# Kernel tuning notes

Hardware: AMD Instinct MI355X
Metric: run time of the kernel (lower is better)

Reference implementation:

```python
import jax, jax.numpy as jnp
import numpy as np

N, C, T, H, W = 2, 512, 8, 28, 28
THW = T * H * W
BN_EPS = 1e-5


def conv1x1(x, Wt, b):
    # pointwise channel mixing, equivalent to 1x1 Conv2d/Conv3d on (N,C,T,H,W)
    return jnp.einsum('oc,ncthw->nothw', Wt, x) + b[None, :, None, None, None]


def setup_inputs() -> dict:
    key = jax.random.key(0)
    ks = jax.random.split(key, 8)
    s = 1.0 / np.sqrt(C)
    x = jax.random.normal(ks[0], (N, C, T, H, W), dtype=jnp.float32)
    mask = jax.random.uniform(ks[1], (N, C, T, H, W), dtype=jnp.float32)
    Wh = jax.random.normal(ks[2], (C, C), dtype=jnp.float32) * s
    Wg = jax.random.normal(ks[3], (C, C), dtype=jnp.float32) * s
    Wm = jax.random.normal(ks[4], (C, C), dtype=jnp.float32) * s
    Wz = jax.random.normal(ks[5], (C, C), dtype=jnp.float32) * s  # kaiming-like
    bh = jnp.zeros((C,), jnp.float32)
    bg = jnp.zeros((C,), jnp.float32)
    bm = jnp.zeros((C,), jnp.float32)
    bz = jnp.zeros((C,), jnp.float32)
    bn_w = jnp.ones((C,), jnp.float32)
    bn_b = jnp.zeros((C,), jnp.float32)
    gamma = jnp.float32(1.0)  # self.gamma (undefined in source __init__); learnable scalar
    return dict(x=x, mask=mask, Wh=Wh, bh=bh, Wg=Wg, bg=bg, Wm=Wm, bm=bm,
                Wz=Wz, bz=bz, bn_w=bn_w, bn_b=bn_b, gamma=gamma)


def reference(x, mask, Wh, bh, Wg, bg, Wm, bm, Wz, bz, bn_w, bn_b, gamma):
    n = x.shape[0]
    # proj_f = h(x) reshaped (N, THW, C); proj_g = g(x) (N, C, THW)
    ph_x = conv1x1(x, Wh, bh).reshape(n, C, THW)
    pg = conv1x1(x, Wg, bg).reshape(n, C, THW)
    # energy[n,t,s] = sum_c ph_x[n,c,t] * pg[n,c,s]  -> (N, THW, THW)
    energy = jnp.einsum('nct,ncs->nts', ph_x, pg)
    attention = jax.nn.softmax(energy, axis=-1)
    # proj_h uses self.h on mask (faithful to source)
    ph_m = conv1x1(mask, Wh, bh).reshape(n, C, THW)
    # bmm(proj_h, attention^T): [n,c,t] = sum_s ph_m[n,c,s] * attention[n,t,s]
    mask_energy = jnp.einsum('ncs,nts->nct', ph_m, attention)
    mask_atten = jax.nn.softmax(mask_energy, axis=-1)  # softmax over THW
    pm = conv1x1(x, Wm, bm)
    out = pm * mask_atten.reshape(n, C, T, H, W)
    # W_z: 1x1 Conv3d + BatchNorm3d (training-mode batch stats, weight=1, bias=0)
    wy = conv1x1(x, Wz, bz)
    mu = jnp.mean(wy, axis=(0, 2, 3, 4), keepdims=True)
    var = jnp.var(wy, axis=(0, 2, 3, 4), keepdims=True)
    wy = (wy - mu) * jax.lax.rsqrt(var + BN_EPS)
    wy = wy * bn_w[None, :, None, None, None] + bn_b[None, :, None, None, None]
    return gamma * out + wy
```

## Files before the change

### kernel.cpp

```cpp
#include <hip/hip_runtime.h>
#include <hip/hip_bf16.h>
#include <math.h>

#define NN 2
#define CC 512
#define PP 6272
#define TCHMAX 1664
#define NCHK 4
#define NJT 49
#define KSP 4
#define EM 64.0f
static const size_t PPC = (size_t)PP * CC;
static const size_t NCP = (size_t)NN * PPC;

typedef unsigned short ushortT;
typedef __attribute__((ext_vector_type(8))) short short8;
typedef __attribute__((ext_vector_type(4))) float f32x4;

__device__ __forceinline__ ushortT f2bf(float f) {
  __hip_bfloat16 h = __float2bfloat16(f);
  return *reinterpret_cast<ushortT*>(&h);
}
__device__ __forceinline__ float bf2f(ushortT u) {
  return __uint_as_float(((unsigned)u) << 16);
}

__device__ __forceinline__ void ld_g2l(const void* g, void* l) {
  __builtin_amdgcn_global_load_lds(
      (const __attribute__((address_space(1))) void*)g,
      (__attribute__((address_space(3))) void*)l, 16, 0, 0);
}

__global__ __launch_bounds__(256) void k_cast4(const float* __restrict__ W0,
                                               const float* __restrict__ W1,
                                               const float* __restrict__ W2,
                                               const float* __restrict__ W3,
                                               ushortT* __restrict__ dst) {
  const float* src = (blockIdx.y == 0) ? W0 : (blockIdx.y == 1) ? W1
                    : (blockIdx.y == 2) ? W2 : W3;
  const int i = (blockIdx.x * 256 + threadIdx.x) * 4;
  float4 v = *(const float4*)&src[i];
  ushort4 o;
  o.x = f2bf(v.x); o.y = f2bf(v.y); o.z = f2bf(v.z); o.w = f2bf(v.w);
  *(ushort4*)&dst[(size_t)blockIdx.y * CC * CC + i] = o;
}

__global__ void k_castT(const float* __restrict__ in, ushortT* __restrict__ out) {
  __shared__ float T[32][33];
  const int p0 = blockIdx.x * 32, c0 = blockIdx.y * 32;
  const int tx = threadIdx.x, ty = threadIdx.y;
  const size_t nbi = (size_t)blockIdx.z * PPC;
#pragma unroll
  for (int i = 0; i < 4; ++i)
    T[ty + i * 8][tx] = in[nbi + (size_t)(c0 + ty + i * 8) * PP + p0 + tx];
  __syncthreads();
#pragma unroll
  for (int i = 0; i < 4; ++i) {
    int r = ty + i * 8;
    out[nbi + (size_t)(p0 + r) * CC + c0 + tx] = f2bf(T[tx][r]);
  }
}

template <int OM>
__global__ __launch_bounds__(256) void k_bgemm(const ushortT* __restrict__ A,
                                               const ushortT* __restrict__ B,
                                               const float* __restrict__ bias,
                                               ushortT* __restrict__ out,
                                               int KD, size_t sAn, size_t sBn,
                                               size_t sOn, int ldo) {
  __shared__ __align__(16) ushortT smem[17408];
  ushortT* At = smem;
  ushortT* Bt = smem + 8192;
  const int tid = threadIdx.x;
  const int l = tid & 63, w = tid >> 6;
  const int j0 = blockIdx.x * 128;
  const int i0 = blockIdx.y * 128;
  A += (size_t)blockIdx.z * sAn;
  B += (size_t)blockIdx.z * sBn;
  out += (size_t)blockIdx.z * sOn;
  const int wi = (w & 1) * 64, wj = (w >> 1) * 64;
  const int lr = l & 15, lk = l >> 4;
  const int sr = l >> 3, scg = l & 7;

  f32x4 acc[4][4] = {};

  for (int k0 = 0; k0 < KD; k0 += 64) {
#pragma unroll
    for (int i = 0; i < 4; ++i) {
      int row = w * 32 + i * 8 + sr;
      int cs = scg ^ (row & 7);
      ld_g2l(A + (size_t)(i0 + row) * KD + k0 + cs * 8, (char*)At + (w * 4 + i) * 1024);
      ld_g2l(B + (size_t)(j0 + row) * KD + k0 + cs * 8, (char*)Bt + (w * 4 + i) * 1024);
    }
    __syncthreads();
#pragma unroll
    for (int ks = 0; ks < 2; ++ks) {
      short8 af[4], bfv[4];
      const int cc = ks * 4 + lk;
#pragma unroll
      for (int tt = 0; tt < 4; ++tt) {
        int row = wi + tt * 16 + lr;
        af[tt] = *(const short8*)((const char*)At + row * 128 + ((cc ^ (row & 7)) * 16));
      }
#pragma unroll
      for (int ss = 0; ss < 4; ++ss) {
        int row = wj + ss * 16 + lr;
        bfv[ss] = *(const short8*)((const char*)Bt + row * 128 + ((cc ^ (row & 7)) * 16));
      }
#pragma unroll
      for (int tt = 0; tt < 4; ++tt)
#pragma unroll
        for (int ss = 0; ss < 4; ++ss)
          acc[tt][ss] = __builtin_amdgcn_mfma_f32_16x16x32_bf16(af[tt], bfv[ss], acc[tt][ss], 0, 0, 0);
    }
    __syncthreads();
  }
  const int r4 = (l >> 4) * 4;
  ushortT (*Tr)[136] = (ushortT(*)[136])smem;
  if (OM == 0) {
    float bj[4];
#pragma unroll
    for (int ss = 0; ss < 4; ++ss) bj[ss] = bias[j0 + wj + ss * 16 + lr];
#pragma unroll
    for (int tt = 0; tt < 4; ++tt)
#pragma unroll
      for (int r = 0; r < 4; ++r) {
        int row = wi + tt * 16 + r4 + r;
#pragma unroll
        for (int ss = 0; ss < 4; ++ss)
          Tr[row][wj + ss * 16 + lr] = f2bf(acc[tt][ss][r] + bj[ss]);
      }
  } else {
#pragma unroll
    for (int tt = 0; tt < 4; ++tt)
#pragma unroll
      for (int r = 0; r < 4; ++r) {
        int row = wi + tt * 16 + r4 + r;
        float bi = bias[i0 + row];
#pragma unroll
        for (int ss = 0; ss < 4; ++ss)
          Tr[row][wj + ss * 16 + lr] = f2bf(acc[tt][ss][r] + bi);
      }
  }
  __syncthreads();
#pragma unroll
  for (int q = 0; q < 8; ++q) {
    int chunk = q * 256 + tid;
    int row = chunk >> 4, cg = chunk & 15;
    short8 v = *(const short8*)&Tr[row][cg * 8];
    *(short8*)&out[(size_t)(i0 + row) * ldo + j0 + cg * 8] = v;
  }
}

__global__ __launch_bounds__(256) void k_energy(const ushortT* __restrict__ phxT,
                                                const ushortT* __restrict__ pgT,
                                                ushortT* __restrict__ Ech,
                                                float* __restrict__ Estat,
                                                int tbase) {
  __shared__ __align__(16) ushortT smem[17408];
  __shared__ float Ss[128][2];
  ushortT* At = smem;
  ushortT* Bt = smem + 8192;
  const int tid = threadIdx.x;
  const int l = tid & 63, w = tid >> 6;
  const int j0 = blockIdx.x * 128;
  const int i0 = blockIdx.y * 128;
  const int z = blockIdx.z;
  const ushortT* A = phxT + (size_t)z * PPC + (size_t)tbase * CC;
  const ushortT* B = pgT + (size_t)z * PPC;
  ushortT* out = Ech + (size_t)z * TCHMAX * PP;
  const int wi = (w & 1) * 64, wj = (w >> 1) * 64;
  const int lr = l & 15, lk = l >> 4;
  const int sr = l >> 3, scg = l & 7;

  f32x4 acc[4][4] = {};

  for (int k0 = 0; k0 < CC; k0 += 64) {
#pragma unroll
    for (int i = 0; i < 4; ++i) {
      int row = w * 32 + i * 8 + sr;
      int cs = scg ^ (row & 7);
      ld_g2l(A + (size_t)(i0 + row) * CC + k0 + cs * 8, (char*)At + (w * 4 + i) * 1024);
      ld_g2l(B + (size_t)(j0 + row) * CC + k0 + cs * 8, (char*)Bt + (w * 4 + i) * 1024);
    }
    __syncthreads();
#pragma unroll
    for (int ks = 0; ks < 2; ++ks) {
      short8 af[4], bfv[4];
      const int cc = ks * 4 + lk;
#pragma unroll
      for (int tt = 0; tt < 4; ++tt) {
        int row = wi + tt * 16 + lr;
        af[tt] = *(const short8*)((const char*)At + row * 128 + ((cc ^ (row & 7)) * 16));
      }
#pragma unroll
      for (int ss = 0; ss < 4; ++ss) {
        int row = wj + ss * 16 + lr;
        bfv[ss] = *(const short8*)((const char*)Bt + row * 128 + ((cc ^ (row & 7)) * 16));
      }
#pragma unroll
      for (int tt = 0; tt < 4; ++tt)
#pragma unroll
        for (int ss = 0; ss < 4; ++ss)
          acc[tt][ss] = __builtin_amdgcn_mfma_f32_16x16x32_bf16(af[tt], bfv[ss], acc[tt][ss], 0, 0, 0);
    }
    __syncthreads();
  }
  const int r4 = (l >> 4) * 4;
  const int jh = w >> 1;
  ushortT (*Tr)[136] = (ushortT(*)[136])smem;
#pragma unroll
  for (int tt = 0; tt < 4; ++tt)
#pragma unroll
    for (int r = 0; r < 4; ++r) {
      int row = wi + tt * 16 + r4 + r;
      float u0 = __expf(acc[tt][0][r] - EM);
      float u1 = __expf(acc[tt][1][r] - EM);
      float u2 = __expf(acc[tt][2][r] - EM);
      float u3 = __expf(acc[tt][3][r] - EM);
      Tr[row][wj + lr]      = f2bf(u0);
      Tr[row][wj + 16 + lr] = f2bf(u1);
      Tr[row][wj + 32 + lr] = f2bf(u2);
      Tr[row][wj + 48 + lr] = f2bf(u3);
      float sx = (u0 + u1) + (u2 + u3);
#pragma unroll
      for (int d = 1; d < 16; d <<= 1) sx += __shfl_xor(sx, d);
      if (lr == 0) Ss[row][jh] = sx;
    }
  __syncthreads();
  if (tid < 128) {
    Estat[((size_t)z * TCHMAX + i0 + tid) * NJT + blockIdx.x] =
        Ss[tid][0] + Ss[tid][1];
  }
#pragma unroll
  for (int q = 0; q < 8; ++q) {
    int chunk = q * 256 + tid;
    int row = chunk >> 4, cg = chunk & 15;
    short8 v = *(const short8*)&Tr[row][cg * 8];
    *(short8*)&out[(size_t)(i0 + row) * PP + j0 + cg * 8] = v;
  }
}

__global__ __launch_bounds__(256) void k_zcomb(const float* __restrict__ Estat,
                                               float* __restrict__ rowZ, int rows) {
  const int r = blockIdx.x * 256 + threadIdx.x;
  if (r >= NN * rows) return;
  const int z = r / rows, tl = r % rows;
  const float* p = Estat + ((size_t)z * TCHMAX + tl) * NJT;
  float s = 0.f;
#pragma unroll
  for (int j = 0; j < NJT; ++j) s += p[j];
  rowZ[z * TCHMAX + tl] = 1.0f / s;
}

__global__ __launch_bounds__(256) void k_me(const ushortT* __restrict__ phmB,
                                            const ushortT* __restrict__ Ech,
                                            ushortT* __restrict__ mePart) {
  __shared__ __align__(16) ushortT smem[12288];
  ushortT* At = smem;
  ushortT* Bt = smem + 8192;
  const int tid = threadIdx.x;
  const int l = tid & 63, w = tid >> 6;
  const int tl0 = blockIdx.x * 64;
  const int c0 = blockIdx.y * 128;
  const int bz = blockIdx.z;
  const int z = bz / KSP, ks = bz % KSP;
  const size_t nb = (size_t)z * PPC;
  const ushortT* Pb = Ech + (size_t)z * TCHMAX * PP;
  const int wc = (w & 1) * 64, wt = (w >> 1) * 32;
  const int lr = l & 15, lk = l >> 4;
  const int sr = l >> 3, scg = l & 7;

  f32x4 acc[4][2] = {};

  const int sBeg = ((ks * 98) / KSP) * 64;
  const int sEnd = (((ks + 1) * 98) / KSP) * 64;
  for (int s0 = sBeg; s0 < sEnd; s0 += 64) {
#pragma unroll
    for (int i = 0; i < 4; ++i) {
      int row = w * 32 + i * 8 + sr;
      int cs = scg ^ (row & 7);
      ld_g2l(phmB + nb + (size_t)(c0 + row) * PP + s0 + cs * 8,
             (char*)At + (w * 4 + i) * 1024);
    }
#pragma unroll
    for (int i = 0; i < 2; ++i) {
      int row = w * 16 + i * 8 + sr;
      int cs = scg ^ (row & 7);
      ld_g2l(Pb + (size_t)(tl0 + row) * PP + s0 + cs * 8,
             (char*)Bt + (w * 2 + i) * 1024);
    }
    __syncthreads();
#pragma unroll
    for (int kk = 0; kk < 2; ++kk) {
      short8 af[4], bfv[2];
      const int cc = kk * 4 + lk;
#pragma unroll
      for (int ct = 0; ct < 4; ++ct) {
        int row = wc + ct * 16 + lr;
        af[ct] = *(const short8*)((const char*)At + row * 128 + ((cc ^ (row & 7)) * 16));
      }
#pragma unroll
      for (int tt = 0; tt < 2; ++tt) {
        int row = wt + tt * 16 + lr;
        bfv[tt] = *(const short8*)((const char*)Bt + row * 128 + ((cc ^ (row & 7)) * 16));
      }
#pragma unroll
      for (int ct = 0; ct < 4; ++ct)
#pragma unroll
        for (int tt = 0; tt < 2; ++tt)
          acc[ct][tt] = __builtin_amdgcn_mfma_f32_16x16x32_bf16(af[ct], bfv[tt], acc[ct][tt], 0, 0, 0);
    }
    __syncthreads();
  }
  const int r4 = (l >> 4) * 4;
  ushortT (*Tr)[72] = (ushortT(*)[72])smem;
#pragma unroll
  for (int ct = 0; ct < 4; ++ct)
#pragma unroll
    for (int r = 0; r < 4; ++r) {
      int row = wc + ct * 16 + r4 + r;
#pragma unroll
      for (int tt = 0; tt < 2; ++tt)
        Tr[row][wt + tt * 16 + lr] = f2bf(acc[ct][tt][r]);
    }
  __syncthreads();
  ushortT* out = mePart + ((size_t)(ks * NN + z) * CC) * TCHMAX;
#pragma unroll
  for (int q = 0; q < 4; ++q) {
    int chunk = q * 256 + tid;
    int row = chunk >> 3, cg = chunk & 7;
    short8 v = *(const short8*)&Tr[row][cg * 8];
    *(short8*)&out[(size_t)(c0 + row) * TCHMAX + tl0 + cg * 8] = v;
  }
}

__global__ __launch_bounds__(256) void k_meadd(const ushortT* __restrict__ mePart,
                                               const float* __restrict__ rowZ,
                                               ushortT* __restrict__ meb,
                                               int tbase, int rows) {
  const int idx = (blockIdx.x * 256 + threadIdx.x) * 4;
  const int tl = idx % rows;
  const int c = (idx / rows) % CC;
  const int z = idx / (rows * CC);
  float s0 = 0.f, s1 = 0.f, s2 = 0.f, s3 = 0.f;
#pragma unroll
  for (int ks = 0; ks < KSP; ++ks) {
    const size_t o = ((size_t)(ks * NN + z) * CC + c) * TCHMAX + tl;
    ushort4 a = *(const ushort4*)&mePart[o];
    s0 += bf2f(a.x); s1 += bf2f(a.y); s2 += bf2f(a.z); s3 += bf2f(a.w);
  }
  const float4 rz = *(const float4*)&rowZ[z * TCHMAX + tl];
  ushort4 v;
  v.x = f2bf(s0 * rz.x); v.y = f2bf(s1 * rz.y);
  v.z = f2bf(s2 * rz.z); v.w = f2bf(s3 * rz.w);
  *(ushort4*)&meb[((size_t)z * CC + c) * PP + tbase + tl] = v;
}

__global__ __launch_bounds__(256) void k_soft2(const ushortT* __restrict__ me,
                                               float* __restrict__ m2,
                                               float* __restrict__ Z2) {
  __shared__ float red[256];
  const ushortT* row = me + (size_t)blockIdx.x * PP;
  const int tid = threadIdx.x;
  const int NCH = PP / 8;
  float m = -INFINITY;
  for (int i = tid; i < NCH; i += 256) {
    short8 v = *(const short8*)&row[i * 8];
#pragma unroll
    for (int j = 0; j < 8; ++j) m = fmaxf(m, bf2f((ushortT)v[j]));
  }
  red[tid] = m;
  __syncthreads();
  for (int s = 128; s > 0; s >>= 1) {
    if (tid < s) red[tid] = fmaxf(red[tid], red[tid + s]);
    __syncthreads();
  }
  m = red[0];
  __syncthreads();
  float zz = 0.f;
  for (int i = tid; i < NCH; i += 256) {
    short8 v = *(const short8*)&row[i * 8];
#pragma unroll
    for (int j = 0; j < 8; ++j) zz += __expf(bf2f((ushortT)v[j]) - m);
  }
  red[tid] = zz;
  __syncthreads();
  for (int s = 128; s > 0; s >>= 1) {
    if (tid < s) red[tid] += red[tid + s];
    __syncthreads();
  }
  if (tid == 0) { m2[blockIdx.x] = m; Z2[blockIdx.x] = red[0]; }
}

__global__ __launch_bounds__(256) void k_bnstat(const ushortT* __restrict__ wz,
                                                float* __restrict__ mu,
                                                float* __restrict__ rinv) {
  __shared__ float rs[256];
  __shared__ float rq[256];
  const int c = blockIdx.x;
  const int tid = threadIdx.x;
  const int NCH = PP / 8;
  float s = 0.f, q = 0.f;
  for (int n = 0; n < NN; ++n) {
    const ushortT* rowp = wz + (size_t)n * CC * PP + (size_t)c * PP;
    for (int i = tid; i < NCH; i += 256) {
      short8 v = *(const short8*)&rowp[i * 8];
#pragma unroll
      for (int j = 0; j < 8; ++j) {
        float f = bf2f((ushortT)v[j]);
        s += f;
        q += f * f;
      }
    }
  }
  rs[tid] = s; rq[tid] = q;
  __syncthreads();
  for (int st = 128; st > 0; st >>= 1) {
    if (tid < st) { rs[tid] += rs[tid + st]; rq[tid] += rq[tid + st]; }
    __syncthreads();
  }
  if (tid == 0) {
    const float inv_n = 1.0f / (float)(NN * PP);
    float mean = rs[0] * inv_n;
    float var = rq[0] * inv_n - mean * mean;
    mu[c] = mean;
    rinv[c] = rsqrtf(var + 1e-5f);
  }
}

__global__ __launch_bounds__(256) void k_final(const ushortT* __restrict__ pmB,
                                               const ushortT* __restrict__ me,
                                               const ushortT* __restrict__ wz,
                                               const float* __restrict__ m2,
                                               const float* __restrict__ Z2,
                                               const float* __restrict__ mu,
                                               const float* __restrict__ rinv,
                                               const float* __restrict__ bnw,
                                               const float* __restrict__ bnb,
                                               const float* __restrict__ gamma,
                                               float* __restrict__ out) {
  const int e4 = blockIdx.x * 256 + threadIdx.x;
  const size_t e = (size_t)e4 * 4;
  const int nc = (int)(e / PP);
  const int c = nc & (CC - 1);
  const float m = m2[nc];
  const float rz = 1.0f / Z2[nc];
  const float mub = mu[c];
  const float ri = rinv[c] * bnw[c];
  const float bb = bnb[c];
  const float g = gamma[0];
  ushort4 pv = *(const ushort4*)&pmB[e];
  ushort4 mev = *(const ushort4*)&me[e];
  ushort4 wzv = *(const ushort4*)&wz[e];
  float4 o;
  o.x = g * bf2f(pv.x) * (__expf(bf2f(mev.x) - m) * rz) + (bf2f(wzv.x) - mub) * ri + bb;
  o.y = g * bf2f(pv.y) * (__expf(bf2f(mev.y) - m) * rz) + (bf2f(wzv.y) - mub) * ri + bb;
  o.z = g * bf2f(pv.z) * (__expf(bf2f(mev.z) - m) * rz) + (bf2f(wzv.z) - mub) * ri + bb;
  o.w = g * bf2f(pv.w) * (__expf(bf2f(mev.w) - m) * rz) + (bf2f(wzv.w) - mub) * ri + bb;
  *(float4*)&out[e] = o;
}

extern "C" void kernel_launch(void* const* d_in, const int* in_sizes, int n_in,
                              void* d_out, int out_size, void* d_ws, size_t ws_size,
                              hipStream_t stream) {
  (void)in_sizes; (void)n_in; (void)out_size; (void)ws_size;
  const float* x    = (const float*)d_in[0];
  const float* mask = (const float*)d_in[1];
  const float* Wh   = (const float*)d_in[2];
  const float* bh   = (const float*)d_in[3];
  const float* Wg   = (const float*)d_in[4];
  const float* bg   = (const float*)d_in[5];
  const float* Wm   = (const float*)d_in[6];
  const float* bm   = (const float*)d_in[7];
  const float* Wz   = (const float*)d_in[8];
  const float* bz   = (const float*)d_in[9];
  const float* bnw  = (const float*)d_in[10];
  const float* bnb  = (const float*)d_in[11];
  const float* gam  = (const float*)d_in[12];

  ushortT* wzb  = (ushortT*)d_ws;
  ushortT* meb  = wzb + NCP;
  ushortT* pmB  = meb + NCP;
  ushortT* phxT = pmB + NCP;
  ushortT* pgT  = phxT + NCP;
  ushortT* phmB = pgT + NCP;
  ushortT* Wbf  = phmB + NCP;
  ushortT* Whbf = Wbf;
  ushortT* Wgbf = Wbf + 1 * CC * CC;
  ushortT* Wmbf = Wbf + 2 * CC * CC;
  ushortT* Wzbf = Wbf + 3 * CC * CC;
  float* m2    = (float*)(Wbf + 4 * CC * CC);
  float* Z2    = m2 + NN * CC;
  float* mu    = Z2 + NN * CC;
  float* rin   = mu + CC;
  float* Estat = rin + CC;
  float* rowZ  = Estat + (size_t)NN * TCHMAX * NJT;
  float* region = rowZ + (size_t)NN * TCHMAX + 16;
  ushortT* xT    = (ushortT*)region;
  ushortT* maskT = xT + NCP;
  ushortT* Ech    = (ushortT*)region;
  ushortT* mePart = Ech + (size_t)NN * TCHMAX * PP;

  k_cast4<<<dim3(256, 4), 256, 0, stream>>>(Wh, Wg, Wm, Wz, Wbf);
  dim3 gct(PP / 32, CC / 32, NN);
  k_castT<<<gct, dim3(32, 8), 0, stream>>>(x, xT);
  k_castT<<<gct, dim3(32, 8), 0, stream>>>(mask, maskT);

  dim3 gPc(CC / 128, PP / 128, NN);
  k_bgemm<0><<<gPc, 256, 0, stream>>>(xT, Whbf, bh, phxT, CC, PPC, 0, PPC, CC);
  k_bgemm<0><<<gPc, 256, 0, stream>>>(xT, Wgbf, bg, pgT, CC, PPC, 0, PPC, CC);
  dim3 gCp(PP / 128, CC / 128, NN);
  k_bgemm<1><<<gCp, 256, 0, stream>>>(Whbf, maskT, bh, phmB, CC, 0, PPC, PPC, PP);
  k_bgemm<1><<<gCp, 256, 0, stream>>>(Wmbf, xT, bm, pmB, CC, 0, PPC, PPC, PP);
  k_bgemm<1><<<gCp, 256, 0, stream>>>(Wzbf, xT, bz, wzb, CC, 0, PPC, PPC, PP);

  static const int chunkTiles[NCHK] = {13, 12, 12, 12};
  int tbase = 0;
  for (int ch = 0; ch < NCHK; ++ch) {
    const int tiles = chunkTiles[ch];
    const int rows = tiles * 128;
    dim3 gE(NJT, tiles, NN);
    k_energy<<<gE, 256, 0, stream>>>(phxT, pgT, Ech, Estat, tbase);
    k_zcomb<<<(NN * rows + 255) / 256, 256, 0, stream>>>(Estat, rowZ, rows);
    dim3 gM(rows / 64, CC / 128, NN * KSP);
    k_me<<<gM, 256, 0, stream>>>(phmB, Ech, mePart);
    k_meadd<<<NN * CC * rows / 1024, 256, 0, stream>>>(mePart, rowZ, meb, tbase, rows);
    tbase += rows;
  }

  k_soft2<<<NN * CC, 256, 0, stream>>>(meb, m2, Z2);
  k_bnstat<<<CC, 256, 0, stream>>>(wzb, mu, rin);
  const int total4 = (int)(NCP / 4);
  k_final<<<total4 / 256, 256, 0, stream>>>(pmB, meb, wzb, m2, Z2, mu, rin,
                                            bnw, bnb, gam, (float*)d_out);
}
```

Baseline: 595.6 us.

## Fuse paired 1x1 conv GEMMs, add XCD-aware block remap, raise k_me split-K

Merges the two projections that share xT (h and g on the P-major side, m and z on the C-major side) into dual-output GEMM kernels, so each input tile is loaded into LDS once for two weight matrices. Adds an XCD-aware workgroup-id remap to the GEMM, energy and mask-energy kernels so neighbouring tiles land on the same XCD and share its L2. Makes the k_me split-K factor a template parameter and uses 8 splits when the workspace is large enough, for more parallelism. The fused kernels double accumulator registers and LDS use, which may reduce occupancy, and the higher split adds partial-sum traffic in k_meadd.

```diff
diff --git a/kernel.cpp b/kernel.cpp
--- a/kernel.cpp
+++ b/kernel.cpp
@@ -8,7 +8,6 @@
 #define TCHMAX 1664
 #define NCHK 4
 #define NJT 49
-#define KSP 4
 #define EM 64.0f
 static const size_t PPC = (size_t)PP * CC;
 static const size_t NCP = (size_t)NN * PPC;
@@ -29,6 +28,12 @@
   __builtin_amdgcn_global_load_lds(
       (const __attribute__((address_space(1))) void*)g,
       (__attribute__((address_space(3))) void*)l, 16, 0, 0);
+}
+
+__device__ __forceinline__ int xcd_remap(int orig, int nwg) {
+  const int q = nwg >> 3, r = nwg & 7;
+  const int x = orig & 7, lo = orig >> 3;
+  return (x < r) ? x * (q + 1) + lo : r * (q + 1) + (x - r) * q + lo;
 }
 
 __global__ __launch_bounds__(256) void k_cast4(const float* __restrict__ W0,
@@ -73,11 +78,17 @@
   ushortT* Bt = smem + 8192;
   const int tid = threadIdx.x;
   const int l = tid & 63, w = tid >> 6;
-  const int j0 = blockIdx.x * 128;
-  const int i0 = blockIdx.y * 128;
-  A += (size_t)blockIdx.z * sAn;
-  B += (size_t)blockIdx.z * sBn;
-  out += (size_t)blockIdx.z * sOn;
+  const int gx = gridDim.x, gy = gridDim.y;
+  const int orig = blockIdx.x + gx * (blockIdx.y + gy * blockIdx.z);
+  const int wgid = xcd_remap(orig, gx * gy * gridDim.z);
+  const int yb = wgid % gy;
+  const int xb = (wgid / gy) % gx;
+  const int zb = wgid / (gy * gx);
+  const int j0 = xb * 128;
+  const int i0 = yb * 128;
+  A += (size_t)zb * sAn;
+  B += (size_t)zb * sBn;
+  out += (size_t)zb * sOn;
   const int wi = (w & 1) * 64, wj = (w >> 1) * 64;
   const int lr = l & 15, lk = l >> 4;
   const int sr = l >> 3, scg = l & 7;
@@ -150,6 +161,188 @@
     short8 v = *(const short8*)&Tr[row][cg * 8];
     *(short8*)&out[(size_t)(i0 + row) * ldo + j0 + cg * 8] = v;
   }
+}
+
+__global__ __launch_bounds__(256) void k_convPC(const ushortT* __restrict__ xTg,
+                                                const ushortT* __restrict__ W1,
+                                                const ushortT* __restrict__ W2,
+                                                const float* __restrict__ b1,
+                                                const float* __restrict__ b2,
+                                                ushortT* __restrict__ o1g,
+                                                ushortT* __restrict__ o2g) {
+  __shared__ __align__(16) ushortT smem[24576];
+  ushortT* At = smem;
+  ushortT* B1t = smem + 8192;
+  ushortT* B2t = smem + 16384;
+  const int tid = threadIdx.x;
+  const int l = tid & 63, w = tid >> 6;
+  const int orig = blockIdx.x + 4 * (blockIdx.y + 49 * blockIdx.z);
+  const int wgid = xcd_remap(orig, 4 * 49 * NN);
+  const int j0 = (wgid & 3) * 128;
+  const int i0 = ((wgid >> 2) % 49) * 128;
+  const int zb = wgid / 196;
+  const ushortT* A = xTg + (size_t)zb * PPC;
+  ushortT* o1 = o1g + (size_t)zb * PPC;
+  ushortT* o2 = o2g + (size_t)zb * PPC;
+  const int wi = (w & 1) * 64, wj = (w >> 1) * 64;
+  const int lr = l & 15, lk = l >> 4;
+  const int sr = l >> 3, scg = l & 7;
+
+  f32x4 acc1[4][4] = {}, acc2[4][4] = {};
+
+  for (int k0 = 0; k0 < CC; k0 += 64) {
+#pragma unroll
+    for (int i = 0; i < 4; ++i) {
+      int row = w * 32 + i * 8 + sr;
+      int cs = scg ^ (row & 7);
+      ld_g2l(A + (size_t)(i0 + row) * CC + k0 + cs * 8, (char*)At + (w * 4 + i) * 1024);
+      ld_g2l(W1 + (size_t)(j0 + row) * CC + k0 + cs * 8, (char*)B1t + (w * 4 + i) * 1024);
+      ld_g2l(W2 + (size_t)(j0 + row) * CC + k0 + cs * 8, (char*)B2t + (w * 4 + i) * 1024);
+    }
+    __syncthreads();
+#pragma unroll
+    for (int ks = 0; ks < 2; ++ks) {
+      short8 af[4], bf1[4], bf2[4];
+      const int cc = ks * 4 + lk;
+#pragma unroll
+      for (int tt = 0; tt < 4; ++tt) {
+        int row = wi + tt * 16 + lr;
+        af[tt] = *(const short8*)((const char*)At + row * 128 + ((cc ^ (row & 7)) * 16));
+      }
+#pragma unroll
+      for (int ss = 0; ss < 4; ++ss) {
+        int row = wj + ss * 16 + lr;
+        bf1[ss] = *(const short8*)((const char*)B1t + row * 128 + ((cc ^ (row & 7)) * 16));
+        bf2[ss] = *(const short8*)((const char*)B2t + row * 128 + ((cc ^ (row & 7)) * 16));
+      }
+#pragma unroll
+      for (int tt = 0; tt < 4; ++tt)
+#pragma unroll
+        for (int ss = 0; ss < 4; ++ss) {
+          acc1[tt][ss] = __builtin_amdgcn_mfma_f32_16x16x32_bf16(af[tt], bf1[ss], acc1[tt][ss], 0, 0, 0);
+          acc2[tt][ss] = __builtin_amdgcn_mfma_f32_16x16x32_bf16(af[tt], bf2[ss], acc2[tt][ss], 0, 0, 0);
+        }
+    }
+    __syncthreads();
+  }
+  const int r4 = (l >> 4) * 4;
+  ushortT (*Tr)[136] = (ushortT(*)[136])smem;
+  auto epi = [&](f32x4 (&acc)[4][4], const float* __restrict__ bsrc,
+                 ushortT* __restrict__ out) {
+    float bj[4];
+#pragma unroll
+    for (int ss = 0; ss < 4; ++ss) bj[ss] = bsrc[j0 + wj + ss * 16 + lr];
+#pragma unroll
+    for (int tt = 0; tt < 4; ++tt)
+#pragma unroll
+      for (int r = 0; r < 4; ++r) {
+        int row = wi + tt * 16 + r4 + r;
+#pragma unroll
+        for (int ss = 0; ss < 4; ++ss)
+          Tr[row][wj + ss * 16 + lr] = f2bf(acc[tt][ss][r] + bj[ss]);
+      }
+    __syncthreads();
+#pragma unroll
+    for (int q = 0; q < 8; ++q) {
+      int chunk = q * 256 + tid;
+      int row = chunk >> 4, cg = chunk & 15;
+      short8 v = *(const short8*)&Tr[row][cg * 8];
+      *(short8*)&out[(size_t)(i0 + row) * CC + j0 + cg * 8] = v;
+    }
+    __syncthreads();
+  };
+  epi(acc1, b1, o1);
+  epi(acc2, b2, o2);
+}
+
+__global__ __launch_bounds__(256) void k_convCP(const ushortT* __restrict__ A1,
+                                                const ushortT* __restrict__ A2,
+                                                const ushortT* __restrict__ xTg,
+                                                const float* __restrict__ b1,
+                                                const float* __restrict__ b2,
+                                                ushortT* __restrict__ o1g,
+                                                ushortT* __restrict__ o2g) {
+  __shared__ __align__(16) ushortT smem[24576];
+  ushortT* A1t = smem;
+  ushortT* A2t = smem + 8192;
+  ushortT* Bt = smem + 16384;
+  const int tid = threadIdx.x;
+  const int l = tid & 63, w = tid >> 6;
+  const int orig = blockIdx.x + 49 * (blockIdx.y + 4 * blockIdx.z);
+  const int wgid = xcd_remap(orig, 4 * 49 * NN);
+  const int i0 = (wgid & 3) * 128;
+  const int j0 = ((wgid >> 2) % 49) * 128;
+  const int zb = wgid / 196;
+  const ushortT* B = xTg + (size_t)zb * PPC;
+  ushortT* o1 = o1g + (size_t)zb * PPC;
+  ushortT* o2 = o2g + (size_t)zb * PPC;
+  const int wi = (w & 1) * 64, wj = (w >> 1) * 64;
+  const int lr = l & 15, lk = l >> 4;
+  const int sr = l >> 3, scg = l & 7;
+
+  f32x4 acc1[4][4] = {}, acc2[4][4] = {};
+
+  for (int k0 = 0; k0 < CC; k0 += 64) {
+#pragma unroll
+    for (int i = 0; i < 4; ++i) {
+      int row = w * 32 + i * 8 + sr;
+      int cs = scg ^ (row & 7);
+      ld_g2l(A1 + (size_t)(i0 + row) * CC + k0 + cs * 8, (char*)A1t + (w * 4 + i) * 1024);
+      ld_g2l(A2 + (size_t)(i0 + row) * CC + k0 + cs * 8, (char*)A2t + (w * 4 + i) * 1024);
+      ld_g2l(B + (size_t)(j0 + row) * CC + k0 + cs * 8, (char*)Bt + (w * 4 + i) * 1024);
+    }
+    __syncthreads();
+#pragma unroll
+    for (int ks = 0; ks < 2; ++ks) {
+      short8 af1[4], af2[4], bfv[4];
+      const int cc = ks * 4 + lk;
+#pragma unroll
+      for (int tt = 0; tt < 4; ++tt) {
+        int row = wi + tt * 16 + lr;
+        af1[tt] = *(const short8*)((const char*)A1t + row * 128 + ((cc ^ (row & 7)) * 16));
+        af2[tt] = *(const short8*)((const char*)A2t + row * 128 + ((cc ^ (row & 7)) * 16));
+      }
+#pragma unroll
+      for (int ss = 0; ss < 4; ++ss) {
+        int row = wj + ss * 16 + lr;
+        bfv[ss] = *(const short8*)((const char*)Bt + row * 128 + ((cc ^ (row & 7)) * 16));
+      }
+#pragma unroll
+      for (int tt = 0; tt < 4; ++tt)
+#pragma unroll
+        for (int ss = 0; ss < 4; ++ss) {
+          acc1[tt][ss] = __builtin_amdgcn_mfma_f32_16x16x32_bf16(af1[tt], bfv[ss], acc1[tt][ss], 0, 0, 0);
+          acc2[tt][ss] = __builtin_amdgcn_mfma_f32_16x16x32_bf16(af2[tt], bfv[ss], acc2[tt][ss], 0, 0, 0);
+        }
+    }
+    __syncthreads();
+  }
+  const int r4 = (l >> 4) * 4;
+  ushortT (*Tr)[136] = (ushortT(*)[136])smem;
+  auto epi = [&](f32x4 (&acc)[4][4], const float* __restrict__ bsrc,
+                 ushortT* __restrict__ out) {
+#pragma unroll
+    for (int tt = 0; tt < 4; ++tt)
+#pragma unroll
+      for (int r = 0; r < 4; ++r) {
+        int row = wi + tt * 16 + r4 + r;
+        float bi = bsrc[i0 + row];
+#pragma unroll
+        for (int ss = 0; ss < 4; ++ss)
+          Tr[row][wj + ss * 16 + lr] = f2bf(acc[tt][ss][r] + bi);
+      }
+    __syncthreads();
+#pragma unroll
+    for (int q = 0; q < 8; ++q) {
+      int chunk = q * 256 + tid;
+      int row = chunk >> 4, cg = chunk & 15;
+      short8 v = *(const short8*)&Tr[row][cg * 8];
+      *(short8*)&out[(size_t)(i0 + row) * PP + j0 + cg * 8] = v;
+    }
+    __syncthreads();
+  };
+  epi(acc1, b1, o1);
+  epi(acc2, b2, o2);
 }
 
 __global__ __launch_bounds__(256) void k_energy(const ushortT* __restrict__ phxT,
@@ -163,9 +356,14 @@
   ushortT* Bt = smem + 8192;
   const int tid = threadIdx.x;
   const int l = tid & 63, w = tid >> 6;
-  const int j0 = blockIdx.x * 128;
-  const int i0 = blockIdx.y * 128;
-  const int z = blockIdx.z;
+  const int tiles = gridDim.y;
+  const int orig = blockIdx.x + NJT * (blockIdx.y + tiles * blockIdx.z);
+  const int wgid = xcd_remap(orig, NJT * tiles * NN);
+  const int it = wgid % tiles;
+  const int jt = (wgid / tiles) % NJT;
+  const int z = wgid / (tiles * NJT);
+  const int j0 = jt * 128;
+  const int i0 = it * 128;
   const ushortT* A = phxT + (size_t)z * PPC + (size_t)tbase * CC;
   const ushortT* B = pgT + (size_t)z * PPC;
   ushortT* out = Ech + (size_t)z * TCHMAX * PP;
@@ -229,8 +427,7 @@
     }
   __syncthreads();
   if (tid < 128) {
-    Estat[((size_t)z * TCHMAX + i0 + tid) * NJT + blockIdx.x] =
-        Ss[tid][0] + Ss[tid][1];
+    Estat[((size_t)z * TCHMAX + i0 + tid) * NJT + jt] = Ss[tid][0] + Ss[tid][1];
   }
 #pragma unroll
   for (int q = 0; q < 8; ++q) {
@@ -253,6 +450,7 @@
   rowZ[z * TCHMAX + tl] = 1.0f / s;
 }
 
+template <int KSPT>
 __global__ __launch_bounds__(256) void k_me(const ushortT* __restrict__ phmB,
                                             const ushortT* __restrict__ Ech,
                                             ushortT* __restrict__ mePart) {
@@ -261,10 +459,16 @@
   ushortT* Bt = smem + 8192;
   const int tid = threadIdx.x;
   const int l = tid & 63, w = tid >> 6;
-  const int tl0 = blockIdx.x * 64;
-  const int c0 = blockIdx.y * 128;
-  const int bz = blockIdx.z;
-  const int z = bz / KSP, ks = bz % KSP;
+  const int gx = gridDim.x;
+  const int orig = blockIdx.x + gx * (blockIdx.y + 4 * blockIdx.z);
+  const int nwg = gx * 4 * (NN * KSPT);
+  const int wgid = (orig & 7) * (nwg >> 3) + (orig >> 3);
+  const int cb = wgid & 3;
+  const int tl = (wgid >> 2) % gx;
+  const int bz = (wgid >> 2) / gx;
+  const int tl0 = tl * 64;
+  const int c0 = cb * 128;
+  const int z = bz / KSPT, ks = bz % KSPT;
   const size_t nb = (size_t)z * PPC;
   const ushortT* Pb = Ech + (size_t)z * TCHMAX * PP;
   const int wc = (w & 1) * 64, wt = (w >> 1) * 32;
@@ -273,8 +477,8 @@
 
   f32x4 acc[4][2] = {};
 
-  const int sBeg = ((ks * 98) / KSP) * 64;
-  const int sEnd = (((ks + 1) * 98) / KSP) * 64;
+  const int sBeg = ((ks * 98) / KSPT) * 64;
+  const int sEnd = (((ks + 1) * 98) / KSPT) * 64;
   for (int s0 = sBeg; s0 < sEnd; s0 += 64) {
 #pragma unroll
     for (int i = 0; i < 4; ++i) {
@@ -335,6 +539,7 @@
   }
 }
 
+template <int KSPT>
 __global__ __launch_bounds__(256) void k_meadd(const ushortT* __restrict__ mePart,
                                                const float* __restrict__ rowZ,
                                                ushortT* __restrict__ meb,
@@ -345,7 +550,7 @@
   const int z = idx / (rows * CC);
   float s0 = 0.f, s1 = 0.f, s2 = 0.f, s3 = 0.f;
 #pragma unroll
-  for (int ks = 0; ks < KSP; ++ks) {
+  for (int ks = 0; ks < KSPT; ++ks) {
     const size_t o = ((size_t)(ks * NN + z) * CC + c) * TCHMAX + tl;
     ushort4 a = *(const ushort4*)&mePart[o];
     s0 += bf2f(a.x); s1 += bf2f(a.y); s2 += bf2f(a.z); s3 += bf2f(a.w);
@@ -464,7 +669,7 @@
 extern "C" void kernel_launch(void* const* d_in, const int* in_sizes, int n_in,
                               void* d_out, int out_size, void* d_ws, size_t ws_size,
                               hipStream_t stream) {
-  (void)in_sizes; (void)n_in; (void)out_size; (void)ws_size;
+  (void)in_sizes; (void)n_in; (void)out_size;
   const float* x    = (const float*)d_in[0];
   const float* mask = (const float*)d_in[1];
   const float* Wh   = (const float*)d_in[2];
@@ -502,18 +707,22 @@
   ushortT* Ech    = (ushortT*)region;
   ushortT* mePart = Ech + (size_t)NN * TCHMAX * PP;
 
+  const size_t regionOffB = (size_t)((char*)region - (char*)d_ws);
+  const size_t need8 = regionOffB +
+      ((size_t)NN * TCHMAX * PP + 8ull * NN * CC * TCHMAX) * 2;
+  const bool k8 = ws_size >= need8;
+
   k_cast4<<<dim3(256, 4), 256, 0, stream>>>(Wh, Wg, Wm, Wz, Wbf);
   dim3 gct(PP / 32, CC / 32, NN);
   k_castT<<<gct, dim3(32, 8), 0, stream>>>(x, xT);
   k_castT<<<gct, dim3(32, 8), 0, stream>>>(mask, maskT);
 
-  dim3 gPc(CC / 128, PP / 128, NN);
-  k_bgemm<0><<<gPc, 256, 0, stream>>>(xT, Whbf, bh, phxT, CC, PPC, 0, PPC, CC);
-  k_bgemm<0><<<gPc, 256, 0, stream>>>(xT, Wgbf, bg, pgT, CC, PPC, 0, PPC, CC);
-  dim3 gCp(PP / 128, CC / 128, NN);
-  k_bgemm<1><<<gCp, 256, 0, stream>>>(Whbf, maskT, bh, phmB, CC, 0, PPC, PPC, PP);
-  k_bgemm<1><<<gCp, 256, 0, stream>>>(Wmbf, xT, bm, pmB, CC, 0, PPC, PPC, PP);
-  k_bgemm<1><<<gCp, 256, 0, stream>>>(Wzbf, xT, bz, wzb, CC, 0, PPC, PPC, PP);
+  k_convPC<<<dim3(CC / 128, PP / 128, NN), 256, 0, stream>>>(
+      xT, Whbf, Wgbf, bh, bg, phxT, pgT);
+  k_bgemm<1><<<dim3(PP / 128, CC / 128, NN), 256, 0, stream>>>(
+      Whbf, maskT, bh, phmB, CC, 0, PPC, PPC, PP);
+  k_convCP<<<dim3(PP / 128, CC / 128, NN), 256, 0, stream>>>(
+      Wmbf, Wzbf, xT, bm, bz, pmB, wzb);
 
   static const int chunkTiles[NCHK] = {13, 12, 12, 12};
   int tbase = 0;
@@ -523,9 +732,17 @@
     dim3 gE(NJT, tiles, NN);
     k_energy<<<gE, 256, 0, stream>>>(phxT, pgT, Ech, Estat, tbase);
     k_zcomb<<<(NN * rows + 255) / 256, 256, 0, stream>>>(Estat, rowZ, rows);
-    dim3 gM(rows / 64, CC / 128, NN * KSP);
-    k_me<<<gM, 256, 0, stream>>>(phmB, Ech, mePart);
-    k_meadd<<<NN * CC * rows / 1024, 256, 0, stream>>>(mePart, rowZ, meb, tbase, rows);
+    if (k8) {
+      dim3 gM(rows / 64, CC / 128, NN * 8);
+      k_me<8><<<gM, 256, 0, stream>>>(phmB, Ech, mePart);
+      k_meadd<8><<<NN * CC * rows / 1024, 256, 0, stream>>>(mePart, rowZ, meb,
+                                                            tbase, rows);
+    } else {
+      dim3 gM(rows / 64, CC / 128, NN * 4);
+      k_me<4><<<gM, 256, 0, stream>>>(phmB, Ech, mePart);
+      k_meadd<4><<<NN * CC * rows / 1024, 256, 0, stream>>>(mePart, rowZ, meb,
+                                                            tbase, rows);
+    }
     tbase += rows;
   }
 
```

Measured after the change: 563.6 us. 1.06x faster.
